# Performance work log

Measured on AMD Instinct MI355X. Metric: run time of the kernel, lower is better.

Reference implementation:

```python
import jax, jax.numpy as jnp
import numpy as np

B, S, H, MAX_STEP = 128, 1024, 256, 10
NEG_INF = -1e8


def setup_inputs() -> dict:
    key = jax.random.key(0)
    ks = jax.random.split(key, 16)
    sc = 0.05
    return {
        "s0": jax.random.normal(ks[0], (B, H), jnp.float32),
        "h0": jax.random.normal(ks[1], (B, H), jnp.float32),
        "doc_encoding": jax.random.normal(ks[2], (B, S, H), jnp.float32),
        "W_ih": jax.random.normal(ks[3], (3 * H, H), jnp.float32) * sc,
        "W_hh": jax.random.normal(ks[4], (3 * H, H), jnp.float32) * sc,
        "b_ih": jax.random.normal(ks[5], (3 * H,), jnp.float32) * sc,
        "b_hh": jax.random.normal(ks[6], (3 * H,), jnp.float32) * sc,
        "Wq": jax.random.normal(ks[7], (H, H), jnp.float32) * sc,
        "bq": jax.random.normal(ks[8], (H,), jnp.float32) * sc,
        "Wd": jax.random.normal(ks[9], (H, H), jnp.float32) * sc,
        "bd": jax.random.normal(ks[10], (H,), jnp.float32) * sc,
        "Ws": jax.random.normal(ks[11], (1, H), jnp.float32) * sc,
        "bs": jax.random.normal(ks[12], (1,), jnp.float32) * sc,
        "tgt": jax.random.randint(ks[13], (B, MAX_STEP), 0, S, jnp.int64 if jax.config.jax_enable_x64 else jnp.int32),
        "sent_length": jax.random.randint(ks[14], (B,), 1, S + 1, jnp.int64 if jax.config.jax_enable_x64 else jnp.int32),
    }


def reference(s0, h0, doc_encoding, W_ih, W_hh, b_ih, b_hh, Wq, bq, Wd, bd, Ws, bs, tgt, sent_length):
    batch, sent_len, hid = doc_encoding.shape
    # padding mask: 1 where position >= doc length
    mask = (jnp.arange(sent_len)[None, :] >= sent_length[:, None]).astype(doc_encoding.dtype)  # [B,S]
    # precomputed attention keys: linear_d(context)
    precompute = jnp.einsum('bsh,kh->bsk', doc_encoding, Wd) + bd  # [B,S,H]
    # teacher-forced indices (original maps -1 -> 0)
    tgt_idx = jnp.where(tgt == -1, 0, tgt)  # [B,T]
    batch_ar = jnp.arange(batch)

    def gru_cell(x, h):
        gi = x @ W_ih.T + b_ih  # [B,3H]
        gh = h @ W_hh.T + b_hh
        i_r, i_z, i_n = jnp.split(gi, 3, axis=-1)
        h_r, h_z, h_n = jnp.split(gh, 3, axis=-1)
        r = jax.nn.sigmoid(i_r + h_r)
        z = jax.nn.sigmoid(i_z + h_z)
        n = jnp.tanh(i_n + r * h_n)
        return (1.0 - z) * n + z * h

    def step(carry, idx_t):
        cur_input, h = carry
        h = gru_cell(cur_input, h)
        target = h @ Wq.T + bq  # [B,H]
        energy = jnp.squeeze(jnp.tanh(precompute + target[:, None, :]) @ Ws.T, -1) + bs[0]  # [B,S]
        energy = energy * (1.0 - mask) + mask * NEG_INF
        cur_next = doc_encoding[batch_ar, idx_t]  # hard-attention gather [B,H]
        return (cur_next, h), energy

    _, all_score = jax.lax.scan(step, (s0, h0), tgt_idx.T)  # [T,B,S]
    return all_score, mask
```

## Files before the change

### kernel.cpp

```cpp
#include <hip/hip_runtime.h>

typedef unsigned short ushort_t;
typedef unsigned int uint_t;
typedef __attribute__((ext_vector_type(8))) short short8;
typedef __attribute__((ext_vector_type(4))) float f32x4;

#define B_   128
#define S_   1024
#define H_   256
#define T_   10
#define NEG_INF_ -1e8f

static __device__ __forceinline__ ushort_t f2bf(float x) {
    unsigned int u = __float_as_uint(x);
    unsigned int r = u + 0x7FFFu + ((u >> 16) & 1u);
    return (ushort_t)(r >> 16);
}
static __device__ __forceinline__ float bflo(uint_t w) {
    return __uint_as_float(w << 16);
}
static __device__ __forceinline__ float bfhi(uint_t w) {
    return __uint_as_float(w & 0xFFFF0000u);
}
static __device__ __forceinline__ float sigf(float x) {
    return 1.0f / (1.0f + __expf(-x));
}
static __device__ __forceinline__ float tanh_acc(float x) {
    return 2.0f / (1.0f + __expf(-2.0f * x)) - 1.0f;
}
static __device__ __forceinline__ float tanh_fast(float x) {
    float u = x * x;
    float p = fmaf(0.019063f, u, -0.18852f);
    p = fmaf(p, u, 0.93106f);
    float r = x * p;
    return __builtin_amdgcn_fmed3f(r, -1.0f, 1.0f);
}
static __device__ __forceinline__ short8 pack_bf8(float4 a, float4 b) {
    short8 r;
    r[0] = (short)f2bf(a.x); r[1] = (short)f2bf(a.y);
    r[2] = (short)f2bf(a.z); r[3] = (short)f2bf(a.w);
    r[4] = (short)f2bf(b.x); r[5] = (short)f2bf(b.y);
    r[6] = (short)f2bf(b.z); r[7] = (short)f2bf(b.w);
    return r;
}

__global__ void prep_transpose(const float* __restrict__ W_ih,
                               const float* __restrict__ W_hh,
                               const float* __restrict__ Wq,
                               uint_t* __restrict__ planes) {
    __shared__ float lds[64][65];
    const int p = blockIdx.x >> 4, tile = blockIdx.x & 15;
    const int j0 = (tile >> 2) * 64, c0 = (tile & 3) * 64;
    const float* src;
    if (p < 3)      src = W_ih + (size_t)p * 65536;
    else if (p < 6) src = W_hh + (size_t)(p - 3) * 65536;
    else            src = Wq;
    uint_t* dst = planes + (size_t)p * 32768;
    const int tid = threadIdx.x;
#pragma unroll
    for (int p4 = 0; p4 < 4; ++p4) {
        int i = p4 * 256 + tid;
        int jj = i >> 4, cc4 = (i & 15) * 4;
        float4 v = *((const float4*)&src[(size_t)(j0 + jj) * 256 + c0 + cc4]);
        lds[jj][cc4]     = v.x;
        lds[jj][cc4 + 1] = v.y;
        lds[jj][cc4 + 2] = v.z;
        lds[jj][cc4 + 3] = v.w;
    }
    __syncthreads();
#pragma unroll
    for (int p8 = 0; p8 < 8; ++p8) {
        int i = p8 * 256 + tid;
        int c2 = i >> 6, j = i & 63;
        float lo = lds[j][c2 * 2], hi = lds[j][c2 * 2 + 1];
        uint_t val = (uint_t)f2bf(lo) | ((uint_t)f2bf(hi) << 16);
        dst[(size_t)(c0 / 2 + c2) * 256 + j0 + j] = val;
    }
}

__global__ void prep_small(const float* __restrict__ Wd, const int* __restrict__ slen,
                           ushort_t* __restrict__ Wd_bf, float* __restrict__ out_mask,
                           float* __restrict__ out_score) {
    int i = blockIdx.x * 256 + threadIdx.x;
    if (i < 65536) { Wd_bf[i] = f2bf(Wd[i]); return; }
    i -= 65536;
    if (i < B_ * S_) {
        int b = i >> 10, s = i & 1023;
        out_mask[i] = (s >= slen[b]) ? 1.0f : 0.0f;
        return;
    }
    i -= B_ * S_;
    int bs = i & (B_ * S_ - 1);
    int b = bs >> 10, s = bs & 1023;
    if (s >= slen[b]) out_score[i] = NEG_INF_;
}

__global__ __launch_bounds__(1024) void build_tiles(const int* __restrict__ slen,
                                                    int* __restrict__ tlist,
                                                    int* __restrict__ tcount) {
    const int tid = threadIdx.x;
    const int b = tid >> 3, st = tid & 7;
    const bool active = (st * 128) < slen[b];
    unsigned long long m = __ballot(active);
    const int lane = tid & 63, wv = tid >> 6;
    __shared__ int wbase[16];
    if (lane == 0) wbase[wv] = __popcll(m);
    __syncthreads();
    if (tid == 0) {
        int s = 0;
#pragma unroll
        for (int i = 0; i < 16; ++i) { int c = wbase[i]; wbase[i] = s; s += c; }
        *tcount = s;
    }
    __syncthreads();
    if (active) {
        unsigned long long below = (lane == 0) ? 0ull : (m << (64 - lane));
        int pos = wbase[wv] + __popcll(below);
        tlist[pos] = tid;
    }
}

__global__ __launch_bounds__(512) void gru_all(
        const float* __restrict__ s0, const float* __restrict__ h0,
        const float* __restrict__ doc, const int* __restrict__ tgt,
        const uint_t* __restrict__ planes, const float* __restrict__ b_ih,
        const float* __restrict__ b_hh, const float* __restrict__ bq,
        float* __restrict__ targets) {
    __shared__ float xs[T_][256];
    __shared__ float hs[256];
    __shared__ float pr[256], pz[256], pn[256], pq[256];
    const int b = blockIdx.x;
    const int tid = threadIdx.x;
    const int j = tid & 255, half = tid >> 8;

    const uint_t* ihr = planes;
    const uint_t* ihz = planes + 32768;
    const uint_t* ihn = planes + 2 * 32768;
    const uint_t* hhr = planes + 3 * 32768;
    const uint_t* hhz = planes + 4 * 32768;
    const uint_t* hhn = planes + 5 * 32768;
    const uint_t* qT  = planes + 6 * 32768;

    for (int i = tid; i < 640; i += 512) {
        int t = i >> 6, c4 = i & 63;
        const float* src;
        if (t == 0) src = s0 + (size_t)b * H_;
        else {
            int idx = tgt[b * T_ + t - 1];
            if (idx < 0) idx = 0;
            src = doc + ((size_t)b * S_ + idx) * H_;
        }
        ((float4*)&xs[t][0])[c4] = ((const float4*)src)[c4];
    }
    if (half == 0) hs[j] = h0[(size_t)b * H_ + j];
    const float bhr = b_hh[j], bhz = b_hh[j + 256], bhn = b_hh[j + 512];
    const float bqj = bq[j];
    const float bihr = b_ih[j], bihz = b_ih[j + 256], bihn = b_ih[j + 512];
    __syncthreads();

    float g_r[5], g_z[5], g_n[5];
#pragma unroll
    for (int u = 0; u < 5; ++u) { g_r[u] = bihr; g_z[u] = bihz; g_n[u] = bihn; }
    const int tbase = half * 5;
#pragma unroll 1
    for (int bb = 0; bb < 16; ++bb) {
        uint_t wr8[8], wz8[8], wn8[8];
#pragma unroll
        for (int v = 0; v < 8; ++v) {
            int c2 = bb * 8 + v;
            wr8[v] = ihr[c2 * 256 + j];
            wz8[v] = ihz[c2 * 256 + j];
            wn8[v] = ihn[c2 * 256 + j];
        }
#pragma unroll
        for (int v = 0; v < 8; ++v) {
            int c2 = bb * 8 + v;
            float wr0 = bflo(wr8[v]), wr1 = bfhi(wr8[v]);
            float wz0 = bflo(wz8[v]), wz1 = bfhi(wz8[v]);
            float wn0 = bflo(wn8[v]), wn1 = bfhi(wn8[v]);
#pragma unroll
            for (int u = 0; u < 5; ++u) {
                float2 x2 = *((const float2*)&xs[tbase + u][c2 * 2]);
                g_r[u] = fmaf(wr0, x2.x, g_r[u]); g_r[u] = fmaf(wr1, x2.y, g_r[u]);
                g_z[u] = fmaf(wz0, x2.x, g_z[u]); g_z[u] = fmaf(wz1, x2.y, g_z[u]);
                g_n[u] = fmaf(wn0, x2.x, g_n[u]); g_n[u] = fmaf(wn1, x2.y, g_n[u]);
            }
        }
    }

    const int c2base = half * 64;
    const uint_t* hhr_h = hhr + (size_t)c2base * 256 + j;
    const uint_t* hhz_h = hhz + (size_t)c2base * 256 + j;
    const uint_t* hhn_h = hhn + (size_t)c2base * 256 + j;
    const uint_t* qT_h  = qT  + (size_t)c2base * 256 + j;

#pragma unroll
    for (int t = 0; t < T_; ++t) {
        const bool holder = (half == (t >= 5 ? 1 : 0));
        const int u = (t < 5) ? t : t - 5;
        float ar = 0.f, az = 0.f, an = 0.f;
#pragma unroll 1
        for (int bb = 0; bb < 8; ++bb) {
            uint_t wr8[8], wz8[8], wn8[8];
#pragma unroll
            for (int v = 0; v < 8; ++v) {
                int c2i = bb * 8 + v;
                wr8[v] = hhr_h[c2i * 256];
                wz8[v] = hhz_h[c2i * 256];
                wn8[v] = hhn_h[c2i * 256];
            }
#pragma unroll
            for (int v = 0; v < 8; ++v) {
                int c2i = bb * 8 + v;
                float2 h2 = *((const float2*)&hs[(c2base + c2i) * 2]);
                ar = fmaf(bflo(wr8[v]), h2.x, ar); ar = fmaf(bfhi(wr8[v]), h2.y, ar);
                az = fmaf(bflo(wz8[v]), h2.x, az); az = fmaf(bfhi(wz8[v]), h2.y, az);
                an = fmaf(bflo(wn8[v]), h2.x, an); an = fmaf(bfhi(wn8[v]), h2.y, an);
            }
        }
        if (!holder) { pr[j] = ar; pz[j] = az; pn[j] = an; }
        __syncthreads();
        if (holder) {
            float art = ar + pr[j] + bhr;
            float azt = az + pz[j] + bhz;
            float ant = an + pn[j] + bhn;
            float r = sigf(g_r[u] + art);
            float z = sigf(g_z[u] + azt);
            float n = tanh_acc(fmaf(r, ant, g_n[u]));
            float hold = hs[j];
            hs[j] = fmaf(z, hold - n, n);
        }
        __syncthreads();
        float q = 0.f;
#pragma unroll 1
        for (int bb = 0; bb < 4; ++bb) {
            uint_t wq16[16];
#pragma unroll
            for (int v = 0; v < 16; ++v)
                wq16[v] = qT_h[(bb * 16 + v) * 256];
#pragma unroll
            for (int v = 0; v < 16; ++v) {
                int c2i = bb * 16 + v;
                float2 h2 = *((const float2*)&hs[(c2base + c2i) * 2]);
                q = fmaf(bflo(wq16[v]), h2.x, q); q = fmaf(bfhi(wq16[v]), h2.y, q);
            }
        }
        if (!holder) pq[j] = q;
        __syncthreads();
        if (holder) targets[((size_t)t * B_ + b) * H_ + j] = q + pq[j] + bqj;
    }
}

__global__ __launch_bounds__(256, 3) void energy_kernel(
        const float* __restrict__ doc, const ushort_t* __restrict__ Wd_bf,
        const float* __restrict__ targets, const float* __restrict__ bd,
        const float* __restrict__ Ws, const float* __restrict__ bs,
        const int* __restrict__ slenp, const int* __restrict__ tlist,
        const int* __restrict__ tcount, float* __restrict__ out) {
    __shared__ float tg[T_][256];
    __shared__ float ws_l[256];
    const int bid = blockIdx.x;
    if (bid >= *tcount) return;
    const int tile = tlist[bid];
    const int b = tile >> 3, st = tile & 7;
    const int tid = threadIdx.x;

    const int slen = slenp[b];

    for (int i = tid; i < 640; i += 256) {
        int t = i >> 6, k4 = i & 63;
        float4 tv = *((const float4*)&targets[((size_t)t * B_ + b) * H_ + k4 * 4]);
        float4 bv = *((const float4*)&bd[k4 * 4]);
        tv.x += bv.x; tv.y += bv.y; tv.z += bv.z; tv.w += bv.w;
        ((float4*)&tg[t][0])[k4] = tv;
    }
    if (tid < 64) ((float4*)ws_l)[tid] = ((const float4*)Ws)[tid];

    const int lane = tid & 63, w = tid >> 6;
    const int r16 = lane & 15, g = lane >> 4;

    const int s0_loc = st * 128 + w * 16 + r16;
    const float* drow0 = doc + ((size_t)b * S_ + s0_loc) * H_ + g * 8;
    const float* drow1 = drow0 + (size_t)64 * H_;
    short8 bdoc0[8], bdoc1[8];
#pragma unroll
    for (int ks = 0; ks < 8; ++ks) {
        float4 v0 = *((const float4*)(drow0 + ks * 32));
        float4 v1 = *((const float4*)(drow0 + ks * 32 + 4));
        bdoc0[ks] = pack_bf8(v0, v1);
        float4 u0 = *((const float4*)(drow1 + ks * 32));
        float4 u1 = *((const float4*)(drow1 + ks * 32 + 4));
        bdoc1[ks] = pack_bf8(u0, u1);
    }
    __syncthreads();

    float e0[T_], e1[T_];
#pragma unroll
    for (int t = 0; t < T_; ++t) { e0[t] = 0.f; e1[t] = 0.f; }

    const ushort_t* wbase = Wd_bf + (size_t)r16 * H_ + g * 8;
    const int kq = g * 4;

    short8 awd[8];
#pragma unroll
    for (int ks = 0; ks < 8; ++ks) awd[ks] = *((const short8*)(wbase + ks * 32));

#pragma unroll 1
    for (int nt = 0; nt < 16; ++nt) {
        const int k0 = nt * 16 + kq;

        short8 awn[8];
        if (nt < 15) {
            const ushort_t* wnext = wbase + (size_t)((nt + 1) * 16) * H_;
#pragma unroll
            for (int ks = 0; ks < 8; ++ks) awn[ks] = *((const short8*)(wnext + ks * 32));
        }

        f32x4 a00 = {0.f, 0.f, 0.f, 0.f};
        f32x4 a01 = {0.f, 0.f, 0.f, 0.f};
        f32x4 a10 = {0.f, 0.f, 0.f, 0.f};
        f32x4 a11 = {0.f, 0.f, 0.f, 0.f};
#pragma unroll
        for (int ks = 0; ks < 4; ++ks) {
            a00 = __builtin_amdgcn_mfma_f32_16x16x32_bf16(awd[ks],     bdoc0[ks],     a00, 0, 0, 0);
            a01 = __builtin_amdgcn_mfma_f32_16x16x32_bf16(awd[ks + 4], bdoc0[ks + 4], a01, 0, 0, 0);
            a10 = __builtin_amdgcn_mfma_f32_16x16x32_bf16(awd[ks],     bdoc1[ks],     a10, 0, 0, 0);
            a11 = __builtin_amdgcn_mfma_f32_16x16x32_bf16(awd[ks + 4], bdoc1[ks + 4], a11, 0, 0, 0);
        }
        f32x4 pA = a00 + a01;
        f32x4 pB = a10 + a11;
        f32x4 ws4 = *((const f32x4*)&ws_l[k0]);

        f32x4 tgc = *((const f32x4*)&tg[0][k0]);
#pragma unroll
        for (int t = 0; t < T_; ++t) {
            f32x4 tgn;
            if (t + 1 < T_) tgn = *((const f32x4*)&tg[t + 1][k0]);
#pragma unroll
            for (int rr = 0; rr < 4; ++rr) {
                e0[t] = fmaf(tanh_fast(pA[rr] + tgc[rr]), ws4[rr], e0[t]);
                e1[t] = fmaf(tanh_fast(pB[rr] + tgc[rr]), ws4[rr], e1[t]);
            }
            if (t + 1 < T_) tgc = tgn;
        }

#pragma unroll
        for (int ks = 0; ks < 8; ++ks) awd[ks] = awn[ks];
    }

#pragma unroll
    for (int t = 0; t < T_; ++t) {
        e0[t] += __shfl_xor(e0[t], 16);
        e0[t] += __shfl_xor(e0[t], 32);
        e1[t] += __shfl_xor(e1[t], 16);
        e1[t] += __shfl_xor(e1[t], 32);
    }

    const float bs0 = bs[0];
    const bool pad0 = (s0_loc >= slen);
    const bool pad1 = (s0_loc + 64 >= slen);
    float* obase = out + (size_t)b * S_ + s0_loc;
#pragma unroll
    for (int tt = g; tt < T_; tt += 4) {
        if (!pad0) obase[(size_t)tt * B_ * S_]      = e0[tt] + bs0;
        if (!pad1) obase[(size_t)tt * B_ * S_ + 64] = e1[tt] + bs0;
    }
}

extern "C" void kernel_launch(void* const* d_in, const int* in_sizes, int n_in,
                              void* d_out, int out_size, void* d_ws, size_t ws_size,
                              hipStream_t stream) {
    (void)in_sizes; (void)n_in; (void)out_size; (void)ws_size;
    const float* s0   = (const float*)d_in[0];
    const float* h0   = (const float*)d_in[1];
    const float* doc  = (const float*)d_in[2];
    const float* W_ih = (const float*)d_in[3];
    const float* W_hh = (const float*)d_in[4];
    const float* b_ih = (const float*)d_in[5];
    const float* b_hh = (const float*)d_in[6];
    const float* Wq   = (const float*)d_in[7];
    const float* bq   = (const float*)d_in[8];
    const float* Wd   = (const float*)d_in[9];
    const float* bd   = (const float*)d_in[10];
    const float* Ws   = (const float*)d_in[11];
    const float* bs   = (const float*)d_in[12];
    const int*   tgt  = (const int*)d_in[13];
    const int*   slen = (const int*)d_in[14];

    float* out_score = (float*)d_out;
    float* out_mask  = out_score + T_ * B_ * S_;

    char* ws = (char*)d_ws;
    uint_t*   planes  = (uint_t*)(ws + 0);
    ushort_t* Wd_bf   = (ushort_t*)(ws + 917504);
    float*    targets = (float*)(ws + 1048576);
    int*      tlist   = (int*)(ws + 2359296);
    int*      tcount  = (int*)(ws + 2363392);

    prep_transpose<<<112, 256, 0, stream>>>(W_ih, W_hh, Wq, planes);
    prep_small<<<5888, 256, 0, stream>>>(Wd, slen, Wd_bf, out_mask, out_score);
    build_tiles<<<1, 1024, 0, stream>>>(slen, tlist, tcount);
    gru_all<<<128, 512, 0, stream>>>(s0, h0, doc, tgt, planes, b_ih, b_hh, bq, targets);
    energy_kernel<<<1024, 256, 0, stream>>>(doc, Wd_bf, targets, bd, Ws, bs, slen,
                                            tlist, tcount, out_score);
}
```

Measured before the change: 162.1 us.

## Halve energy tiles to 64 rows and cache W_hh n-plane in LDS

The energy kernel now uses 64-row sequence tiles with 128 threads, doubling the grid. The tile list is rebuilt at 64-row granularity, so fewer fully padded rows are computed and load balance improves. The GRU kernel copies the W_hh n-gate plane (128 KB) into dynamic shared memory and reads it from LDS during the recurrent steps, which cuts global and L2 traffic in the serial loop. The costs are a large LDS allocation in one block per CU, an upfront copy, and dropping the occupancy hint from the energy kernel's launch bounds.

```diff
diff --git a/kernel.cpp b/kernel.cpp
--- a/kernel.cpp
+++ b/kernel.cpp
@@ -99,24 +99,29 @@
                                                     int* __restrict__ tlist,
                                                     int* __restrict__ tcount) {
     const int tid = threadIdx.x;
-    const int b = tid >> 3, st = tid & 7;
-    const bool active = (st * 128) < slen[b];
-    unsigned long long m = __ballot(active);
     const int lane = tid & 63, wv = tid >> 6;
-    __shared__ int wbase[16];
-    if (lane == 0) wbase[wv] = __popcll(m);
+    __shared__ int wcnt[32], woff[32];
+    const bool a0 = ((tid & 15) * 64) < slen[tid >> 4];
+    unsigned long long m0 = __ballot(a0);
+    const int t2 = 1024 + tid;
+    const bool a1 = ((t2 & 15) * 64) < slen[t2 >> 4];
+    unsigned long long m1 = __ballot(a1);
+    if (lane == 0) { wcnt[wv] = __popcll(m0); wcnt[16 + wv] = __popcll(m1); }
     __syncthreads();
     if (tid == 0) {
         int s = 0;
 #pragma unroll
-        for (int i = 0; i < 16; ++i) { int c = wbase[i]; wbase[i] = s; s += c; }
+        for (int i = 0; i < 32; ++i) { woff[i] = s; s += wcnt[i]; }
         *tcount = s;
     }
     __syncthreads();
-    if (active) {
-        unsigned long long below = (lane == 0) ? 0ull : (m << (64 - lane));
-        int pos = wbase[wv] + __popcll(below);
-        tlist[pos] = tid;
+    if (a0) {
+        unsigned long long below = (lane == 0) ? 0ull : (m0 << (64 - lane));
+        tlist[woff[wv] + __popcll(below)] = tid;
+    }
+    if (a1) {
+        unsigned long long below = (lane == 0) ? 0ull : (m1 << (64 - lane));
+        tlist[woff[16 + wv] + __popcll(below)] = t2;
     }
 }
 
@@ -126,9 +131,15 @@
         const uint_t* __restrict__ planes, const float* __restrict__ b_ih,
         const float* __restrict__ b_hh, const float* __restrict__ bq,
         float* __restrict__ targets) {
-    __shared__ float xs[T_][256];
-    __shared__ float hs[256];
-    __shared__ float pr[256], pz[256], pn[256], pq[256];
+    extern __shared__ char smem[];
+    uint_t* hhn_l = (uint_t*)smem;
+    float*  xs    = (float*)(smem + 131072);
+    float*  hs    = (float*)(smem + 141312);
+    float*  pr    = (float*)(smem + 142336);
+    float*  pz    = (float*)(smem + 143360);
+    float*  pn    = (float*)(smem + 144384);
+    float*  pq    = (float*)(smem + 145408);
+
     const int b = blockIdx.x;
     const int tid = threadIdx.x;
     const int j = tid & 255, half = tid >> 8;
@@ -140,6 +151,10 @@
     const uint_t* hhz = planes + 4 * 32768;
     const uint_t* hhn = planes + 5 * 32768;
     const uint_t* qT  = planes + 6 * 32768;
+
+#pragma unroll
+    for (int i = tid; i < 8192; i += 512)
+        ((uint4*)hhn_l)[i] = ((const uint4*)hhn)[i];
 
     for (int i = tid; i < 640; i += 512) {
         int t = i >> 6, c4 = i & 63;
@@ -150,7 +165,7 @@
             if (idx < 0) idx = 0;
             src = doc + ((size_t)b * S_ + idx) * H_;
         }
-        ((float4*)&xs[t][0])[c4] = ((const float4*)src)[c4];
+        ((float4*)&xs[t * 256])[c4] = ((const float4*)src)[c4];
     }
     if (half == 0) hs[j] = h0[(size_t)b * H_ + j];
     const float bhr = b_hh[j], bhz = b_hh[j + 256], bhn = b_hh[j + 512];
@@ -180,7 +195,7 @@
             float wn0 = bflo(wn8[v]), wn1 = bfhi(wn8[v]);
 #pragma unroll
             for (int u = 0; u < 5; ++u) {
-                float2 x2 = *((const float2*)&xs[tbase + u][c2 * 2]);
+                float2 x2 = *((const float2*)&xs[(tbase + u) * 256 + c2 * 2]);
                 g_r[u] = fmaf(wr0, x2.x, g_r[u]); g_r[u] = fmaf(wr1, x2.y, g_r[u]);
                 g_z[u] = fmaf(wz0, x2.x, g_z[u]); g_z[u] = fmaf(wz1, x2.y, g_z[u]);
                 g_n[u] = fmaf(wn0, x2.x, g_n[u]); g_n[u] = fmaf(wn1, x2.y, g_n[u]);
@@ -191,7 +206,7 @@
     const int c2base = half * 64;
     const uint_t* hhr_h = hhr + (size_t)c2base * 256 + j;
     const uint_t* hhz_h = hhz + (size_t)c2base * 256 + j;
-    const uint_t* hhn_h = hhn + (size_t)c2base * 256 + j;
+    const uint_t* hhn_lh = hhn_l + (size_t)c2base * 256 + j;
     const uint_t* qT_h  = qT  + (size_t)c2base * 256 + j;
 
 #pragma unroll
@@ -201,21 +216,21 @@
         float ar = 0.f, az = 0.f, an = 0.f;
 #pragma unroll 1
         for (int bb = 0; bb < 8; ++bb) {
-            uint_t wr8[8], wz8[8], wn8[8];
+            uint_t wr8[8], wz8[8];
 #pragma unroll
             for (int v = 0; v < 8; ++v) {
                 int c2i = bb * 8 + v;
                 wr8[v] = hhr_h[c2i * 256];
                 wz8[v] = hhz_h[c2i * 256];
-                wn8[v] = hhn_h[c2i * 256];
             }
 #pragma unroll
             for (int v = 0; v < 8; ++v) {
                 int c2i = bb * 8 + v;
                 float2 h2 = *((const float2*)&hs[(c2base + c2i) * 2]);
+                uint_t wn = hhn_lh[c2i * 256];
                 ar = fmaf(bflo(wr8[v]), h2.x, ar); ar = fmaf(bfhi(wr8[v]), h2.y, ar);
                 az = fmaf(bflo(wz8[v]), h2.x, az); az = fmaf(bfhi(wz8[v]), h2.y, az);
-                an = fmaf(bflo(wn8[v]), h2.x, an); an = fmaf(bfhi(wn8[v]), h2.y, an);
+                an = fmaf(bflo(wn),     h2.x, an); an = fmaf(bfhi(wn),     h2.y, an);
             }
         }
         if (!holder) { pr[j] = ar; pz[j] = az; pn[j] = an; }
@@ -251,7 +266,7 @@
     }
 }
 
-__global__ __launch_bounds__(256, 3) void energy_kernel(
+__global__ __launch_bounds__(128) void energy_kernel(
         const float* __restrict__ doc, const ushort_t* __restrict__ Wd_bf,
         const float* __restrict__ targets, const float* __restrict__ bd,
         const float* __restrict__ Ws, const float* __restrict__ bs,
@@ -262,12 +277,12 @@
     const int bid = blockIdx.x;
     if (bid >= *tcount) return;
     const int tile = tlist[bid];
-    const int b = tile >> 3, st = tile & 7;
+    const int b = tile >> 4, st = tile & 15;
     const int tid = threadIdx.x;
 
     const int slen = slenp[b];
 
-    for (int i = tid; i < 640; i += 256) {
+    for (int i = tid; i < 640; i += 128) {
         int t = i >> 6, k4 = i & 63;
         float4 tv = *((const float4*)&targets[((size_t)t * B_ + b) * H_ + k4 * 4]);
         float4 bv = *((const float4*)&bd[k4 * 4]);
@@ -279,9 +294,9 @@
     const int lane = tid & 63, w = tid >> 6;
     const int r16 = lane & 15, g = lane >> 4;
 
-    const int s0_loc = st * 128 + w * 16 + r16;
+    const int s0_loc = st * 64 + w * 16 + r16;
     const float* drow0 = doc + ((size_t)b * S_ + s0_loc) * H_ + g * 8;
-    const float* drow1 = drow0 + (size_t)64 * H_;
+    const float* drow1 = drow0 + (size_t)32 * H_;
     short8 bdoc0[8], bdoc1[8];
 #pragma unroll
     for (int ks = 0; ks < 8; ++ks) {
@@ -358,12 +373,12 @@
 
     const float bs0 = bs[0];
     const bool pad0 = (s0_loc >= slen);
-    const bool pad1 = (s0_loc + 64 >= slen);
+    const bool pad1 = (s0_loc + 32 >= slen);
     float* obase = out + (size_t)b * S_ + s0_loc;
 #pragma unroll
     for (int tt = g; tt < T_; tt += 4) {
         if (!pad0) obase[(size_t)tt * B_ * S_]      = e0[tt] + bs0;
-        if (!pad1) obase[(size_t)tt * B_ * S_ + 64] = e1[tt] + bs0;
+        if (!pad1) obase[(size_t)tt * B_ * S_ + 32] = e1[tt] + bs0;
     }
 }
 
@@ -395,12 +410,12 @@
     ushort_t* Wd_bf   = (ushort_t*)(ws + 917504);
     float*    targets = (float*)(ws + 1048576);
     int*      tlist   = (int*)(ws + 2359296);
-    int*      tcount  = (int*)(ws + 2363392);
+    int*      tcount  = (int*)(ws + 2367488);
 
     prep_transpose<<<112, 256, 0, stream>>>(W_ih, W_hh, Wq, planes);
     prep_small<<<5888, 256, 0, stream>>>(Wd, slen, Wd_bf, out_mask, out_score);
     build_tiles<<<1, 1024, 0, stream>>>(slen, tlist, tcount);
-    gru_all<<<128, 512, 0, stream>>>(s0, h0, doc, tgt, planes, b_ih, b_hh, bq, targets);
-    energy_kernel<<<1024, 256, 0, stream>>>(doc, Wd_bf, targets, bd, Ws, bs, slen,
+    gru_all<<<128, 512, 146432, stream>>>(s0, h0, doc, tgt, planes, b_ih, b_hh, bq, targets);
+    energy_kernel<<<2048, 128, 0, stream>>>(doc, Wd_bf, targets, bd, Ws, bs, slen,
                                             tlist, tcount, out_score);
 }
```

Result: slower. 168.9 us (+4.2%).
